# Optimization experiments

Hardware: AMD Instinct MI355X
Metric: run time of the kernel (lower is better)

The kernel has to match this reference:

```python
import jax, jax.numpy as jnp
import numpy as np

N_NODES = 100000
N_EDGES = 1600000
IN_FEAT = 128
HEADS = 4
OUT_FEAT = 16
ALPHA = 0.2  # LeakyReLU negative slope


def setup_inputs() -> dict:
    key = jax.random.key(0)
    k1, k2, k3, k4, k5 = jax.random.split(key, 5)
    x = jax.random.normal(k1, (N_NODES, IN_FEAT), dtype=jnp.float32)
    edge_index = jax.random.randint(k2, (2, N_EDGES), 0, N_NODES, dtype=jnp.int64)
    # xavier_uniform with gain=1.414
    gain = 1.414
    lim_W = gain * np.sqrt(6.0 / (IN_FEAT + HEADS * OUT_FEAT))
    W = jax.random.uniform(k3, (IN_FEAT, HEADS * OUT_FEAT), minval=-lim_W, maxval=lim_W, dtype=jnp.float32)
    lim_a = gain * np.sqrt(6.0 / (HEADS + OUT_FEAT))
    a_src = jax.random.uniform(k4, (HEADS, OUT_FEAT), minval=-lim_a, maxval=lim_a, dtype=jnp.float32)
    a_dst = jax.random.uniform(k5, (HEADS, OUT_FEAT), minval=-lim_a, maxval=lim_a, dtype=jnp.float32)
    return {"x": x, "edge_index": edge_index, "W": W, "a_src": a_src, "a_dst": a_dst}


def reference(x, edge_index, W, a_src, a_dst):
    N = x.shape[0]
    H, F = a_src.shape
    src, dst = edge_index[0], edge_index[1]

    h = (x @ W).reshape(N, H, F)                 # [N, H, F]
    att_src = jnp.sum(h * a_src, axis=-1)        # [N, H]
    att_dst = jnp.sum(h * a_dst, axis=-1)        # [N, H]

    e = jax.nn.leaky_relu(att_src[src] + att_dst[dst], negative_slope=ALPHA)  # [E, H]

    # segment softmax over edges grouped by dst
    e_max = jax.ops.segment_max(e, dst, num_segments=N)   # [N, H]
    e_max = jnp.where(jnp.isfinite(e_max), e_max, 0.0)    # nodes with no in-edges
    ex = jnp.exp(e - e_max[dst])                           # [E, H]
    denom = jax.ops.segment_sum(ex, dst, num_segments=N)  # [N, H]
    alpha = ex / (denom[dst] + 1e-16)                      # [E, H]
    # dropout: inference mode (training=False) -> identity

    messages = h[src] * alpha[:, :, None]                  # [E, H, F]
    out = jax.ops.segment_sum(messages, dst, num_segments=N)  # [N, H, F]

    out = out.reshape(N, H * F)  # concat=True
    out = jax.nn.elu(out)
    return out
```

## Files before the change

kernel.cpp:

```cpp
#include <hip/hip_runtime.h>


#define NEG_SLOPE 0.2f
#define BSHIFT 9
#define BNODES 512
#define CH 2048

typedef __bf16 bf16x8 __attribute__((ext_vector_type(8)));
typedef float  f32x4  __attribute__((ext_vector_type(4)));

static __device__ __forceinline__ unsigned f2b(float f) {
    union { float f; unsigned u; } v; v.f = f;
    return (v.u + 0x7fffu + ((v.u >> 16) & 1u)) >> 16;
}
static __device__ __forceinline__ float u2f(unsigned u) {
    union { unsigned u32; float f; } v; v.u32 = u; return v.f;
}

__global__ __launch_bounds__(256) void gemm_att_kernel(
    const float* __restrict__ x,
    const float* __restrict__ W,
    const float* __restrict__ a_src,
    const float* __restrict__ a_dst,
    unsigned short* __restrict__ h_out,
    float* __restrict__ att_s_o,
    float* __restrict__ att_d_o,
    int N)
{
    __shared__ bf16x8 Wswz[16][64];
    int t = threadIdx.x;
    for (int i = t; i < 8192; i += 256) {
        int k = i >> 6, n = i & 63;
        __bf16* dp = (__bf16*)&Wswz[((n >> 4) << 2) | (k >> 5)]
                                   [(((k >> 3) & 3) << 4) | (n & 15)];
        dp[k & 7] = (__bf16)W[i];
    }
    __syncthreads();

    int wave = t >> 6;
    int lane = t & 63;
    int col = lane & 15, quad = lane >> 4;
    int node_base = (blockIdx.x * 4 + wave) * 16;
    int arow = min(node_base + col, N - 1);
    const float* xp = x + arow * 128;

    bf16x8 af[4];
    #pragma unroll
    for (int tt = 0; tt < 4; ++tt) {
        float4 xa = *(const float4*)(xp + tt * 32 + quad * 8);
        float4 xb = *(const float4*)(xp + tt * 32 + quad * 8 + 4);
        bf16x8 f;
        f[0] = (__bf16)xa.x; f[1] = (__bf16)xa.y;
        f[2] = (__bf16)xa.z; f[3] = (__bf16)xa.w;
        f[4] = (__bf16)xb.x; f[5] = (__bf16)xb.y;
        f[6] = (__bf16)xb.z; f[7] = (__bf16)xb.w;
        af[tt] = f;
    }

    f32x4 acc[4];
    #pragma unroll
    for (int cb = 0; cb < 4; ++cb) {
        acc[cb] = (f32x4){0.f, 0.f, 0.f, 0.f};
        #pragma unroll
        for (int tt = 0; tt < 4; ++tt)
            acc[cb] = __builtin_amdgcn_mfma_f32_16x16x32_bf16(
                af[tt], Wswz[(cb << 2) | tt][lane], acc[cb], 0, 0, 0);
    }

    #pragma unroll
    for (int cb = 0; cb < 4; ++cb) {
        float ws_ = a_src[cb * 16 + col];
        float wd_ = a_dst[cb * 16 + col];
        #pragma unroll
        for (int r = 0; r < 4; ++r) {
            float v = acc[cb][r];
            int node = node_base + quad * 4 + r;
            float s = v * ws_, d = v * wd_;
            #pragma unroll
            for (int m = 1; m < 16; m <<= 1) {
                s += __shfl_xor(s, m, 64);
                d += __shfl_xor(d, m, 64);
            }
            if (node < N) {
                h_out[node * 64 + cb * 16 + col] = (unsigned short)f2b(v);
                if (col == 0) {
                    att_s_o[(node << 2) | cb] = s;
                    att_d_o[(node << 2) | cb] = d;
                }
            }
        }
    }
}

__global__ __launch_bounds__(256) void bcount_kernel(
    const int* __restrict__ dst, int* __restrict__ bucketCount, int E)
{
    __shared__ int c[256];
    int t = threadIdx.x;
    c[t] = 0;
    __syncthreads();
    for (int e = blockIdx.x * 256 + t; e < E; e += gridDim.x * 256)
        atomicAdd(&c[dst[e] >> BSHIFT], 1);
    __syncthreads();
    if (c[t]) atomicAdd(&bucketCount[t], c[t]);
}

__global__ __launch_bounds__(256) void bscan_kernel(
    const int* __restrict__ bucketCount, int* __restrict__ bucketBase,
    int* __restrict__ bucketCursor, int nb, int E)
{
    __shared__ int sm[256];
    int t = threadIdx.x;
    int v = (t < nb) ? bucketCount[t] : 0;
    sm[t] = v;
    __syncthreads();
    #pragma unroll
    for (int off = 1; off < 256; off <<= 1) {
        int u = (t >= off) ? sm[t - off] : 0;
        __syncthreads();
        sm[t] += u;
        __syncthreads();
    }
    int excl = sm[t] - v;
    if (t <= nb) bucketBase[t] = (t == nb) ? E : excl;
    bucketCursor[t] = (t < nb) ? excl : 0;
}

__global__ __launch_bounds__(256) void bscatter_kernel(
    const int* __restrict__ src, const int* __restrict__ dst,
    int* __restrict__ bucketCursor, int* __restrict__ pairs, int E)
{
    __shared__ int cnt[256], lo[256], gpos[256], cur[256], sm[256];
    __shared__ int2 staged[CH];
    int t = threadIdx.x;
    int base = blockIdx.x * CH;
    int nloc = min(CH, E - base);

    cnt[t] = 0;
    __syncthreads();
    for (int i = t; i < nloc; i += 256)
        atomicAdd(&cnt[dst[base + i] >> BSHIFT], 1);
    __syncthreads();

    int v = cnt[t];
    sm[t] = v;
    __syncthreads();
    #pragma unroll
    for (int off = 1; off < 256; off <<= 1) {
        int u = (t >= off) ? sm[t - off] : 0;
        __syncthreads();
        sm[t] += u;
        __syncthreads();
    }
    lo[t] = sm[t] - v;
    cur[t] = lo[t];
    gpos[t] = (v > 0) ? atomicAdd(&bucketCursor[t], v) : 0;
    __syncthreads();

    for (int i = t; i < nloc; i += 256) {
        int d = dst[base + i];
        int s = src[base + i];
        int b = d >> BSHIFT;
        int k = atomicAdd(&cur[b], 1);
        staged[k] = make_int2((s << BSHIFT) | (d & (BNODES - 1)), b);
    }
    __syncthreads();

    for (int i = t; i < nloc; i += 256) {
        int2 p = staged[i];
        pairs[gpos[p.y] + (i - lo[p.y])] = p.x;
    }
}

__global__ __launch_bounds__(1024) void csrfill_kernel(
    const int* __restrict__ pairs, const int* __restrict__ bucketBase,
    int* __restrict__ rowstart, int* __restrict__ elsrc, int N, int E)
{
    __shared__ int hist[512], cur[512], sm[512];
    int b = blockIdx.x, t = threadIdx.x;
    int node_lo = b << BSHIFT;
    int nn = min(BNODES, N - node_lo);
    int ebase = bucketBase[b];
    int ecnt = bucketBase[b + 1] - ebase;

    if (t < 512) hist[t] = 0;
    __syncthreads();
    for (int i = t; i < ecnt; i += 1024)
        atomicAdd(&hist[pairs[ebase + i] & (BNODES - 1)], 1);
    __syncthreads();

    int v = (t < 512) ? hist[t] : 0;
    if (t < 512) sm[t] = v;
    __syncthreads();
    #pragma unroll
    for (int off = 1; off < 512; off <<= 1) {
        int u = (t >= off && t < 512) ? sm[t - off] : 0;
        __syncthreads();
        if (t < 512) sm[t] += u;
        __syncthreads();
    }
    if (t < 512) {
        int excl = sm[t] - v;
        cur[t] = excl;
        if (t < nn) rowstart[node_lo + t] = ebase + excl;
    }
    if (b == gridDim.x - 1 && t == 0) rowstart[N] = E;
    __syncthreads();

    for (int i = t; i < ecnt; i += 1024) {
        int p = pairs[ebase + i];
        int k = atomicAdd(&cur[p & (BNODES - 1)], 1);
        elsrc[ebase + k] = p >> BSHIFT;
    }
}

__global__ __launch_bounds__(256) void agg_kernel(
    const int* __restrict__ elsrc,
    const int* __restrict__ rowstart,
    const float* __restrict__ att_s,
    const float* __restrict__ att_d,
    const unsigned short* __restrict__ hmat,
    float* __restrict__ out,
    int N)
{
    int node = blockIdx.x * 4 + (threadIdx.x >> 6);
    if (node >= N) return;
    int lane = threadIdx.x & 63;
    int q = lane & 7;
    int eslot = lane >> 3;
    int h = q >> 1;

    int beg = rowstart[node];
    int deg = rowstart[node + 1] - beg;
    float ad = att_d[(node << 2) | h];

    float a0 = 0.f, a1 = 0.f, a2 = 0.f, a3 = 0.f;
    float a4 = 0.f, a5 = 0.f, a6 = 0.f, a7 = 0.f, l = 0.f;

    for (int base = 0; base < deg; base += 8) {
        int e = base + eslot;
        int idx = beg + min(e, deg - 1);
        int s = elsrc[idx];
        float av = att_s[(s << 2) | h] + ad;
        av = fmaxf(av, NEG_SLOPE * av);
        float w = (e < deg) ? __expf(av) : 0.f;
        l += w;
        uint4 hp = *(const uint4*)(hmat + (s << 6) + (q << 3));
        a0 = fmaf(w, u2f(hp.x << 16), a0);
        a1 = fmaf(w, u2f(hp.x & 0xffff0000u), a1);
        a2 = fmaf(w, u2f(hp.y << 16), a2);
        a3 = fmaf(w, u2f(hp.y & 0xffff0000u), a3);
        a4 = fmaf(w, u2f(hp.z << 16), a4);
        a5 = fmaf(w, u2f(hp.z & 0xffff0000u), a5);
        a6 = fmaf(w, u2f(hp.w << 16), a6);
        a7 = fmaf(w, u2f(hp.w & 0xffff0000u), a7);
    }

    #pragma unroll
    for (int m = 8; m <= 32; m <<= 1) {
        a0 += __shfl_xor(a0, m, 64);
        a1 += __shfl_xor(a1, m, 64);
        a2 += __shfl_xor(a2, m, 64);
        a3 += __shfl_xor(a3, m, 64);
        a4 += __shfl_xor(a4, m, 64);
        a5 += __shfl_xor(a5, m, 64);
        a6 += __shfl_xor(a6, m, 64);
        a7 += __shfl_xor(a7, m, 64);
        l  += __shfl_xor(l,  m, 64);
    }

    if (eslot == 0) {
        float rl = 1.0f / (l + 1e-16f);
        float4 v0, v1;
        v0.x = a0 * rl; v0.x = (v0.x > 0.f) ? v0.x : (__expf(v0.x) - 1.f);
        v0.y = a1 * rl; v0.y = (v0.y > 0.f) ? v0.y : (__expf(v0.y) - 1.f);
        v0.z = a2 * rl; v0.z = (v0.z > 0.f) ? v0.z : (__expf(v0.z) - 1.f);
        v0.w = a3 * rl; v0.w = (v0.w > 0.f) ? v0.w : (__expf(v0.w) - 1.f);
        v1.x = a4 * rl; v1.x = (v1.x > 0.f) ? v1.x : (__expf(v1.x) - 1.f);
        v1.y = a5 * rl; v1.y = (v1.y > 0.f) ? v1.y : (__expf(v1.y) - 1.f);
        v1.z = a6 * rl; v1.z = (v1.z > 0.f) ? v1.z : (__expf(v1.z) - 1.f);
        v1.w = a7 * rl; v1.w = (v1.w > 0.f) ? v1.w : (__expf(v1.w) - 1.f);
        float* op = out + (node << 6) + (q << 3);
        *(float4*)op = v0;
        *(float4*)(op + 4) = v1;
    }
}

extern "C" void kernel_launch(void* const* d_in, const int* in_sizes, int n_in,
                              void* d_out, int out_size, void* d_ws, size_t ws_size,
                              hipStream_t stream) {
    const float* x     = (const float*)d_in[0];
    const int*   ei    = (const int*)d_in[1];
    const float* W     = (const float*)d_in[2];
    const float* a_src = (const float*)d_in[3];
    const float* a_dst = (const float*)d_in[4];

    int N = in_sizes[0] / 128;
    int E = in_sizes[1] / 2;
    const int* src = ei;
    const int* dst = ei + E;
    int nb = (N + BNODES - 1) / BNODES;

    char* ws = (char*)d_ws;
    size_t off = 0;
    unsigned short* hmat = (unsigned short*)(ws + off); off += (size_t)N * 64 * 2;
    float* att_s = (float*)(ws + off);  off += (size_t)N * 4 * 4;
    float* att_d = (float*)(ws + off);  off += (size_t)N * 4 * 4;
    int* rowstart = (int*)(ws + off);   off += (size_t)(N + 1) * 4;
    int* elsrc    = (int*)(ws + off);   off += (size_t)E * 4;
    int* pairs    = (int*)(ws + off);   off += (size_t)E * 4;
    int* bucketBase   = (int*)(ws + off); off += 260 * 4;
    int* bucketCursor = (int*)(ws + off); off += 256 * 4;
    int* bucketCount  = (int*)(ws + off); off += 256 * 4;

    hipMemsetAsync(bucketCount, 0, 256 * 4, stream);

    int blocks1 = (N + 63) / 64;
    gemm_att_kernel<<<blocks1, 256, 0, stream>>>(x, W, a_src, a_dst,
                                                 hmat, att_s, att_d, N);

    bcount_kernel<<<512, 256, 0, stream>>>(dst, bucketCount, E);
    bscan_kernel<<<1, 256, 0, stream>>>(bucketCount, bucketBase, bucketCursor, nb, E);

    int blocksS = (E + CH - 1) / CH;
    bscatter_kernel<<<blocksS, 256, 0, stream>>>(src, dst, bucketCursor, pairs, E);

    csrfill_kernel<<<nb, 1024, 0, stream>>>(pairs, bucketBase, rowstart, elsrc, N, E);

    int blocksA = (N + 3) / 4;
    agg_kernel<<<blocksA, 256, 0, stream>>>(elsrc, rowstart, att_s, att_d,
                                            hmat, (float*)d_out, N);
}
```

Baseline: 237.8 us.

## Fuse bucket count into GEMM launch, fold attention vectors into W, drop scan kernel

The bucket-count work now runs as extra blocks inside the GEMM launch, which removes one kernel launch. The standalone bucket scan kernel is removed; the scatter and CSR-fill kernels each redo the 256-entry prefix scan locally from the bucket counts. The attention projections are precomputed as W·a columns and computed with an extra MFMA, which replaces the per-element shuffle reductions. The cost is redundant scans in every block and the a-vector products now being rounded to bf16.

New measurement: 224.2 us. 1.06x faster.

```diff
diff --git a/kernel.cpp b/kernel.cpp
--- a/kernel.cpp
+++ b/kernel.cpp
@@ -5,6 +5,7 @@
 #define BSHIFT 9
 #define BNODES 512
 #define CH 2048
+#define BCB 512
 
 typedef __bf16 bf16x8 __attribute__((ext_vector_type(8)));
 typedef float  f32x4  __attribute__((ext_vector_type(4)));
@@ -25,15 +26,43 @@
     unsigned short* __restrict__ h_out,
     float* __restrict__ att_s_o,
     float* __restrict__ att_d_o,
-    int N)
+    const int* __restrict__ dst,
+    int* __restrict__ bucketCount,
+    int N, int E, int gemmBlocks)
 {
-    __shared__ bf16x8 Wswz[16][64];
+    __shared__ bf16x8 Wswz[20][64];
+    __shared__ int c[256];
     int t = threadIdx.x;
+
+    if (blockIdx.x >= gemmBlocks) {
+        int bid = blockIdx.x - gemmBlocks;
+        c[t] = 0;
+        __syncthreads();
+        for (int e = bid * 256 + t; e < E; e += BCB * 256)
+            atomicAdd(&c[dst[e] >> BSHIFT], 1);
+        __syncthreads();
+        if (c[t]) atomicAdd(&bucketCount[t], c[t]);
+        return;
+    }
+
     for (int i = t; i < 8192; i += 256) {
         int k = i >> 6, n = i & 63;
         __bf16* dp = (__bf16*)&Wswz[((n >> 4) << 2) | (k >> 5)]
                                    [(((k >> 3) & 3) << 4) | (n & 15)];
         dp[k & 7] = (__bf16)W[i];
+    }
+    for (int i = t; i < 1024; i += 256) {
+        int k = i >> 3, c7 = i & 7;
+        int hd = c7 & 3;
+        const float* aa = (c7 < 4) ? a_src : a_dst;
+        float sum = 0.f;
+        #pragma unroll
+        for (int f = 0; f < 16; ++f)
+            sum = fmaf(W[k * 64 + hd * 16 + f], aa[hd * 16 + f], sum);
+        __bf16* dp = (__bf16*)&Wswz[16 + (k >> 5)][(((k >> 3) & 3) << 4) | c7];
+        dp[k & 7] = (__bf16)sum;
+        __bf16* dz = (__bf16*)&Wswz[16 + (k >> 5)][(((k >> 3) & 3) << 4) | (8 + c7)];
+        dz[k & 7] = (__bf16)0.f;
     }
     __syncthreads();
 
@@ -57,7 +86,7 @@
         af[tt] = f;
     }
 
-    f32x4 acc[4];
+    f32x4 acc[4], accA;
     #pragma unroll
     for (int cb = 0; cb < 4; ++cb) {
         acc[cb] = (f32x4){0.f, 0.f, 0.f, 0.f};
@@ -66,77 +95,46 @@
             acc[cb] = __builtin_amdgcn_mfma_f32_16x16x32_bf16(
                 af[tt], Wswz[(cb << 2) | tt][lane], acc[cb], 0, 0, 0);
     }
+    accA = (f32x4){0.f, 0.f, 0.f, 0.f};
+    #pragma unroll
+    for (int tt = 0; tt < 4; ++tt)
+        accA = __builtin_amdgcn_mfma_f32_16x16x32_bf16(
+            af[tt], Wswz[16 + tt][lane], accA, 0, 0, 0);
 
     #pragma unroll
     for (int cb = 0; cb < 4; ++cb) {
-        float ws_ = a_src[cb * 16 + col];
-        float wd_ = a_dst[cb * 16 + col];
         #pragma unroll
         for (int r = 0; r < 4; ++r) {
-            float v = acc[cb][r];
             int node = node_base + quad * 4 + r;
-            float s = v * ws_, d = v * wd_;
-            #pragma unroll
-            for (int m = 1; m < 16; m <<= 1) {
-                s += __shfl_xor(s, m, 64);
-                d += __shfl_xor(d, m, 64);
-            }
+            if (node < N)
+                h_out[node * 64 + cb * 16 + col] = (unsigned short)f2b(acc[cb][r]);
+        }
+    }
+    if (col < 8) {
+        #pragma unroll
+        for (int r = 0; r < 4; ++r) {
+            int node = node_base + quad * 4 + r;
             if (node < N) {
-                h_out[node * 64 + cb * 16 + col] = (unsigned short)f2b(v);
-                if (col == 0) {
-                    att_s_o[(node << 2) | cb] = s;
-                    att_d_o[(node << 2) | cb] = d;
-                }
+                if (col < 4) att_s_o[(node << 2) | col] = accA[r];
+                else         att_d_o[(node << 2) | (col - 4)] = accA[r];
             }
         }
     }
 }
 
-__global__ __launch_bounds__(256) void bcount_kernel(
-    const int* __restrict__ dst, int* __restrict__ bucketCount, int E)
-{
-    __shared__ int c[256];
-    int t = threadIdx.x;
-    c[t] = 0;
-    __syncthreads();
-    for (int e = blockIdx.x * 256 + t; e < E; e += gridDim.x * 256)
-        atomicAdd(&c[dst[e] >> BSHIFT], 1);
-    __syncthreads();
-    if (c[t]) atomicAdd(&bucketCount[t], c[t]);
-}
-
-__global__ __launch_bounds__(256) void bscan_kernel(
-    const int* __restrict__ bucketCount, int* __restrict__ bucketBase,
-    int* __restrict__ bucketCursor, int nb, int E)
-{
-    __shared__ int sm[256];
-    int t = threadIdx.x;
-    int v = (t < nb) ? bucketCount[t] : 0;
-    sm[t] = v;
-    __syncthreads();
-    #pragma unroll
-    for (int off = 1; off < 256; off <<= 1) {
-        int u = (t >= off) ? sm[t - off] : 0;
-        __syncthreads();
-        sm[t] += u;
-        __syncthreads();
-    }
-    int excl = sm[t] - v;
-    if (t <= nb) bucketBase[t] = (t == nb) ? E : excl;
-    bucketCursor[t] = (t < nb) ? excl : 0;
-}
-
 __global__ __launch_bounds__(256) void bscatter_kernel(
     const int* __restrict__ src, const int* __restrict__ dst,
-    int* __restrict__ bucketCursor, int* __restrict__ pairs, int E)
+    const int* __restrict__ bucketCount,
+    int* __restrict__ bucketCursor, int* __restrict__ pairs, int nb, int E)
 {
-    __shared__ int cnt[256], lo[256], gpos[256], cur[256], sm[256];
+    __shared__ int cnt[256], lo[256], gpos[256], cur[256], sm[256], gbc[256];
     __shared__ int2 staged[CH];
     int t = threadIdx.x;
     int base = blockIdx.x * CH;
     int nloc = min(CH, E - base);
 
     cnt[t] = 0;
+    gbc[t] = (t < nb) ? bucketCount[t] : 0;
     __syncthreads();
     for (int i = t; i < nloc; i += 256)
         atomicAdd(&cnt[dst[base + i] >> BSHIFT], 1);
@@ -154,7 +152,19 @@
     }
     lo[t] = sm[t] - v;
     cur[t] = lo[t];
-    gpos[t] = (v > 0) ? atomicAdd(&bucketCursor[t], v) : 0;
+    __syncthreads();
+
+    int g = gbc[t];
+    sm[t] = g;
+    __syncthreads();
+    #pragma unroll
+    for (int off = 1; off < 256; off <<= 1) {
+        int u = (t >= off) ? sm[t - off] : 0;
+        __syncthreads();
+        sm[t] += u;
+        __syncthreads();
+    }
+    gpos[t] = (v > 0) ? (sm[t] - g) + atomicAdd(&bucketCursor[t], v) : 0;
     __syncthreads();
 
     for (int i = t; i < nloc; i += 256) {
@@ -173,18 +183,27 @@
 }
 
 __global__ __launch_bounds__(1024) void csrfill_kernel(
-    const int* __restrict__ pairs, const int* __restrict__ bucketBase,
-    int* __restrict__ rowstart, int* __restrict__ elsrc, int N, int E)
+    const int* __restrict__ pairs, const int* __restrict__ bucketCount,
+    int* __restrict__ rowstart, int* __restrict__ elsrc, int nb, int N, int E)
 {
-    __shared__ int hist[512], cur[512], sm[512];
+    __shared__ int hist[512], cur[512], sm[512], gbc[256], gsm[256];
     int b = blockIdx.x, t = threadIdx.x;
     int node_lo = b << BSHIFT;
     int nn = min(BNODES, N - node_lo);
-    int ebase = bucketBase[b];
-    int ecnt = bucketBase[b + 1] - ebase;
-
+
+    if (t < 256) { gbc[t] = (t < nb) ? bucketCount[t] : 0; gsm[t] = gbc[t]; }
     if (t < 512) hist[t] = 0;
     __syncthreads();
+    #pragma unroll
+    for (int off = 1; off < 256; off <<= 1) {
+        int u = (t >= off && t < 256) ? gsm[t - off] : 0;
+        __syncthreads();
+        if (t < 256) gsm[t] += u;
+        __syncthreads();
+    }
+    int ebase = gsm[b] - gbc[b];
+    int ecnt = gbc[b];
+
     for (int i = t; i < ecnt; i += 1024)
         atomicAdd(&hist[pairs[ebase + i] & (BNODES - 1)], 1);
     __syncthreads();
@@ -309,23 +328,22 @@
     int* rowstart = (int*)(ws + off);   off += (size_t)(N + 1) * 4;
     int* elsrc    = (int*)(ws + off);   off += (size_t)E * 4;
     int* pairs    = (int*)(ws + off);   off += (size_t)E * 4;
-    int* bucketBase   = (int*)(ws + off); off += 260 * 4;
+    int* bucketCount  = (int*)(ws + off); off += 256 * 4;
     int* bucketCursor = (int*)(ws + off); off += 256 * 4;
-    int* bucketCount  = (int*)(ws + off); off += 256 * 4;
-
-    hipMemsetAsync(bucketCount, 0, 256 * 4, stream);
-
-    int blocks1 = (N + 63) / 64;
-    gemm_att_kernel<<<blocks1, 256, 0, stream>>>(x, W, a_src, a_dst,
-                                                 hmat, att_s, att_d, N);
-
-    bcount_kernel<<<512, 256, 0, stream>>>(dst, bucketCount, E);
-    bscan_kernel<<<1, 256, 0, stream>>>(bucketCount, bucketBase, bucketCursor, nb, E);
+
+    hipMemsetAsync(bucketCount, 0, 512 * 4, stream);
+
+    int gemmBlocks = (N + 63) / 64;
+    gemm_att_kernel<<<gemmBlocks + BCB, 256, 0, stream>>>(
+        x, W, a_src, a_dst, hmat, att_s, att_d, dst, bucketCount,
+        N, E, gemmBlocks);
 
     int blocksS = (E + CH - 1) / CH;
-    bscatter_kernel<<<blocksS, 256, 0, stream>>>(src, dst, bucketCursor, pairs, E);
-
-    csrfill_kernel<<<nb, 1024, 0, stream>>>(pairs, bucketBase, rowstart, elsrc, N, E);
+    bscatter_kernel<<<blocksS, 256, 0, stream>>>(src, dst, bucketCount,
+                                                 bucketCursor, pairs, nb, E);
+
+    csrfill_kernel<<<nb, 1024, 0, stream>>>(pairs, bucketCount,
+                                            rowstart, elsrc, nb, N, E);
 
     int blocksA = (N + 3) / 4;
     agg_kernel<<<blocksA, 256, 0, stream>>>(elsrc, rowstart, att_s, att_d,
```
